# Optimization experiments

Measured on AMD Instinct MI355X. Metric: run time of the kernel, lower is better.

Reference implementation:

```python
import jax, jax.numpy as jnp
import numpy as np

EPS = 1e-6

def _log_g(x):
    # log of continuous g(x) = where(x>=0, x+0.5, sigmoid(x)) from minGRU paper
    return jnp.where(x >= 0, jnp.log(jax.nn.relu(x) + 0.5), -jax.nn.softplus(-x))

def setup_inputs() -> dict:
    key = jax.random.key(0)
    ks = jax.random.split(key, 4)
    B, S, D, E = 4, 2048, 1024, 8
    scale = D ** -0.5
    return {
        "inputs": jax.random.normal(ks[0], (B, S, D), dtype=jnp.float32),
        "norm_weight": jnp.ones((D,), jnp.float32),
        "router_w": jax.random.normal(ks[1], (E, D), jnp.float32) * scale,
        "router_b": jnp.zeros((E,), jnp.float32),
        "w_hg": jax.random.normal(ks[2], (E, 2 * D, D), jnp.float32) * scale,
        "w_out": jax.random.normal(ks[3], (E, D, D), jnp.float32) * scale,
    }

def reference(inputs, norm_weight, router_w, router_b, w_hg, w_out):
    D = inputs.shape[-1]
    # --- RMSNorm ---
    x = inputs * jax.lax.rsqrt(jnp.mean(inputs * inputs, axis=-1, keepdims=True) + EPS) * norm_weight
    # --- SMEAR: per-sample soft merge of expert weights via mean-pooled routing ---
    probs = jax.nn.softmax(jnp.mean(x, axis=1) @ router_w.T + router_b, axis=-1)  # [B,E]
    W_hg = jnp.einsum('be,ekd->bkd', probs, w_hg)    # [B,2D,D] merged to_hidden_and_gate
    W_out = jnp.einsum('be,eod->bod', probs, w_out)  # [B,D,D]  merged to_out
    # --- minGRU with merged weights (log-space parallel scan, no initial state) ---
    hg = jnp.einsum('bsd,bkd->bsk', x, W_hg)         # [B,S,2D]
    hidden, gate = hg[..., :D], hg[..., D:]
    log_coeffs = -jax.nn.softplus(gate)                      # log(1 - z_t)
    log_values = -jax.nn.softplus(-gate) + _log_g(hidden)    # log z_t + log g(h~_t)
    a_star = jnp.cumsum(log_coeffs, axis=1)
    log_h = a_star + jax.lax.cumlogsumexp(log_values - a_star, axis=1)
    h = jnp.exp(log_h)                               # [B,S,D] recurrent states
    new_state = h[:, -1:]                            # [B,1,D]
    out = jnp.einsum('bsk,bok->bso', h, W_out)       # proj_out
    aux_loss = jnp.zeros((), inputs.dtype)
    return (out + inputs, new_state, aux_loss)
```

## Files before the change

### kernel.cpp

```cpp
#include <hip/hip_runtime.h>
#include <hip/hip_bf16.h>
#include <hip/hip_fp16.h>

#define B_  4
#define S_  2048
#define D_  1024
#define E_  8
#define K2_ 2048

#define CHUNKS 64
#define CLEN   32

typedef __attribute__((ext_vector_type(8))) short short8;
typedef __attribute__((ext_vector_type(4))) float floatx4;

__device__ __forceinline__ void gld16(const void* g, const void* l) {
    __builtin_amdgcn_global_load_lds(
        (const __attribute__((address_space(1))) unsigned int*)g,
        (__attribute__((address_space(3))) unsigned int*)l, 16, 0, 0);
}

__device__ __forceinline__ unsigned short f2bf(float f) {
    unsigned int u = __float_as_uint(f);
    u += 0x7fffu + ((u >> 16) & 1u);
    return (unsigned short)(u >> 16);
}

__global__ void rmsnorm_k(const float* __restrict__ in, const float* __restrict__ nw,
                          __hip_bfloat16* __restrict__ x) {
    int b = blockIdx.y, s = blockIdx.x, t = threadIdx.x;
    const float4* row = (const float4*)(in + ((size_t)b * S_ + s) * D_);
    float4 v = row[t];
    float ss = v.x * v.x + v.y * v.y + v.z * v.z + v.w * v.w;
#pragma unroll
    for (int o = 32; o > 0; o >>= 1) ss += __shfl_down(ss, o, 64);
    __shared__ float ls[4];
    if ((t & 63) == 0) ls[t >> 6] = ss;
    __syncthreads();
    float tot = ls[0] + ls[1] + ls[2] + ls[3];
    float rs = rsqrtf(tot * (1.0f / (float)D_) + 1e-6f);
    float4 w = ((const float4*)nw)[t];
    ushort4 o;
    o.x = f2bf(v.x * rs * w.x); o.y = f2bf(v.y * rs * w.y);
    o.z = f2bf(v.z * rs * w.z); o.w = f2bf(v.w * rs * w.w);
    ((ushort4*)(x + ((size_t)b * S_ + s) * D_))[t] = o;
}

__global__ void xsum_k(const __hip_bfloat16* __restrict__ x, float* __restrict__ xs) {
    int d = blockIdx.x * 256 + threadIdx.x;
    int b = blockIdx.y;
    int s0 = blockIdx.z * 128;
    const __hip_bfloat16* p = x + ((size_t)b * S_ + s0) * D_ + d;
    float acc = 0.0f;
#pragma unroll 4
    for (int s = 0; s < 128; s++) { acc += __bfloat162float(*p); p += D_; }
    atomicAdd(&xs[b * D_ + d], acc);
}

__global__ void router_k(const float* __restrict__ xs, const float* __restrict__ rw,
                         const float* __restrict__ rb, float* __restrict__ probs,
                         float* __restrict__ aux) {
    int t = threadIdx.x;
    if (t == 255) *aux = 0.0f;
    int pair = t >> 3, sub = t & 7;
    int b = pair >> 3, e = pair & 7;
    float acc = 0.0f;
#pragma unroll 8
    for (int d = sub; d < D_; d += 8) acc += xs[b * D_ + d] * rw[e * D_ + d];
#pragma unroll
    for (int o = 4; o > 0; o >>= 1) acc += __shfl_down(acc, o, 8);
    __shared__ float lg[32];
    if (sub == 0) lg[pair] = acc * (1.0f / (float)S_) + rb[e];
    __syncthreads();
    if (t < 4) {
        float m = -1e30f;
        for (int e2 = 0; e2 < 8; e2++) m = fmaxf(m, lg[t * 8 + e2]);
        float ssum = 0.0f; float ex[8];
        for (int e2 = 0; e2 < 8; e2++) { ex[e2] = expf(lg[t * 8 + e2] - m); ssum += ex[e2]; }
        for (int e2 = 0; e2 < 8; e2++) probs[t * 8 + e2] = ex[e2] / ssum;
    }
}

__global__ void mix_k(const float* __restrict__ probs, const float* __restrict__ whg_e,
                      const float* __restrict__ wout_e, __hip_bfloat16* __restrict__ Whg,
                      __hip_bfloat16* __restrict__ Wout) {
    __shared__ float P[32];
    int t = threadIdx.x;
    if (t < 32) P[t] = probs[t];
    __syncthreads();
    size_t i4 = (size_t)blockIdx.x * 256 + t;
    const size_t T1q = (size_t)K2_ * D_ / 4;
    const size_t T2q = (size_t)D_ * D_ / 4;
    float4 a0 = {0,0,0,0}, a1 = {0,0,0,0}, a2 = {0,0,0,0}, a3 = {0,0,0,0};
    if (i4 < T1q) {
        const float4* src = (const float4*)whg_e;
#pragma unroll
        for (int e = 0; e < 8; e++) {
            float4 wv = src[(size_t)e * T1q + i4];
            float p0 = P[e], p1 = P[8 + e], p2 = P[16 + e], p3 = P[24 + e];
            a0.x += p0 * wv.x; a0.y += p0 * wv.y; a0.z += p0 * wv.z; a0.w += p0 * wv.w;
            a1.x += p1 * wv.x; a1.y += p1 * wv.y; a1.z += p1 * wv.z; a1.w += p1 * wv.w;
            a2.x += p2 * wv.x; a2.y += p2 * wv.y; a2.z += p2 * wv.z; a2.w += p2 * wv.w;
            a3.x += p3 * wv.x; a3.y += p3 * wv.y; a3.z += p3 * wv.z; a3.w += p3 * wv.w;
        }
        ushort4* dst = (ushort4*)Whg;
        ushort4 o;
        o.x = f2bf(a0.x); o.y = f2bf(a0.y); o.z = f2bf(a0.z); o.w = f2bf(a0.w);
        dst[0 * T1q + i4] = o;
        o.x = f2bf(a1.x); o.y = f2bf(a1.y); o.z = f2bf(a1.z); o.w = f2bf(a1.w);
        dst[1 * T1q + i4] = o;
        o.x = f2bf(a2.x); o.y = f2bf(a2.y); o.z = f2bf(a2.z); o.w = f2bf(a2.w);
        dst[2 * T1q + i4] = o;
        o.x = f2bf(a3.x); o.y = f2bf(a3.y); o.z = f2bf(a3.z); o.w = f2bf(a3.w);
        dst[3 * T1q + i4] = o;
    } else {
        size_t j4 = i4 - T1q;
        const float4* src = (const float4*)wout_e;
#pragma unroll
        for (int e = 0; e < 8; e++) {
            float4 wv = src[(size_t)e * T2q + j4];
            float p0 = P[e], p1 = P[8 + e], p2 = P[16 + e], p3 = P[24 + e];
            a0.x += p0 * wv.x; a0.y += p0 * wv.y; a0.z += p0 * wv.z; a0.w += p0 * wv.w;
            a1.x += p1 * wv.x; a1.y += p1 * wv.y; a1.z += p1 * wv.z; a1.w += p1 * wv.w;
            a2.x += p2 * wv.x; a2.y += p2 * wv.y; a2.z += p2 * wv.z; a2.w += p2 * wv.w;
            a3.x += p3 * wv.x; a3.y += p3 * wv.y; a3.z += p3 * wv.z; a3.w += p3 * wv.w;
        }
        ushort4* dst = (ushort4*)Wout;
        ushort4 o;
        o.x = f2bf(a0.x); o.y = f2bf(a0.y); o.z = f2bf(a0.z); o.w = f2bf(a0.w);
        dst[0 * T2q + j4] = o;
        o.x = f2bf(a1.x); o.y = f2bf(a1.y); o.z = f2bf(a1.z); o.w = f2bf(a1.w);
        dst[1 * T2q + j4] = o;
        o.x = f2bf(a2.x); o.y = f2bf(a2.y); o.z = f2bf(a2.z); o.w = f2bf(a2.w);
        dst[2 * T2q + j4] = o;
        o.x = f2bf(a3.x); o.y = f2bf(a3.y); o.z = f2bf(a3.z); o.w = f2bf(a3.w);
        dst[3 * T2q + j4] = o;
    }
}

__global__ __launch_bounds__(512, 2) void gemm_hg_cv(
    const __hip_bfloat16* __restrict__ A, const __hip_bfloat16* __restrict__ Bm,
    __half2* __restrict__ cv) {
    const int K = D_;
    int bz = blockIdx.z;
    A  += (size_t)bz * S_ * D_;
    Bm += (size_t)bz * K2_ * D_;
    __half2* CV = cv + (size_t)bz * S_ * D_;
    int id = blockIdx.x;
    int sw = (id & 7) * 8 + (id >> 3);
    int m0 = (sw >> 3) * 256, n0 = (sw & 7) * 128;
    __shared__ __hip_bfloat16 lA[2][2][256][32];
    __shared__ __hip_bfloat16 lBh[2][2][128][32];
    __shared__ __hip_bfloat16 lBg[2][2][128][32];
    int t = threadIdx.x;
    int w = t >> 6, lane = t & 63;
    int lm = lane & 15, quad = lane >> 4;
    int wr = w >> 1, wc = w & 1;
    floatx4 acch[4][4] = {};
    floatx4 accg[4][4] = {};
    int rloc = lane >> 2;
    int swz4 = ((lane & 3) ^ ((lane >> 3) & 3)) * 16;
    int pch  = (quad ^ ((lm >> 1) & 3)) * 16;

    const __hip_bfloat16* Bh = Bm;
    const __hip_bfloat16* Bg = Bm + (size_t)D_ * K;

    const char* pA0 = (const char*)(A  + (size_t)(m0 + (w * 2 + 0) * 16 + rloc) * K) + swz4;
    const char* pA1 = (const char*)(A  + (size_t)(m0 + (w * 2 + 1) * 16 + rloc) * K) + swz4;
    const char* pBhp = (const char*)(Bh + (size_t)(n0 + w * 16 + rloc) * K) + swz4;
    const char* pBgp = (const char*)(Bg + (size_t)(n0 + w * 16 + rloc) * K) + swz4;

    auto stage_kh0 = [&](int bb) {
        gld16(pA0, &lA[bb][0][(w * 2 + 0) * 16][0]);
        gld16(pA1, &lA[bb][0][(w * 2 + 1) * 16][0]);
        gld16(pBhp, &lBh[bb][0][w * 16][0]);
        gld16(pBgp, &lBg[bb][0][w * 16][0]);
    };
    auto stage_kh1 = [&](int bb) {
        gld16(pA0 + 64, &lA[bb][1][(w * 2 + 0) * 16][0]);
        gld16(pA1 + 64, &lA[bb][1][(w * 2 + 1) * 16][0]);
        gld16(pBhp + 64, &lBh[bb][1][w * 16][0]);
        gld16(pBgp + 64, &lBg[bb][1][w * 16][0]);
        pA0 += 128; pA1 += 128; pBhp += 128; pBgp += 128;
    };

    stage_kh0(0); stage_kh1(0);
    for (int kt = 0; kt < 16; kt++) {
        int cur = kt & 1, nxt = cur ^ 1;
        bool pre = (kt < 15);
        asm volatile("s_waitcnt vmcnt(4)" ::: "memory");
        __builtin_amdgcn_s_barrier();
        short8 af[4], bh0[2], bg0[2];
#pragma unroll
        for (int i = 0; i < 4; i++)
            af[i] = *(const short8*)((const char*)&lA[cur][0][wr * 64 + i * 16 + lm][0] + pch);
#pragma unroll
        for (int jj = 0; jj < 2; jj++) {
            bh0[jj] = *(const short8*)((const char*)&lBh[cur][0][wc * 64 + jj * 16 + lm][0] + pch);
            bg0[jj] = *(const short8*)((const char*)&lBg[cur][0][wc * 64 + jj * 16 + lm][0] + pch);
        }
        if (pre) stage_kh0(nxt);
        asm volatile("s_waitcnt lgkmcnt(0)" ::: "memory");
        __builtin_amdgcn_sched_barrier(0);
        __builtin_amdgcn_s_setprio(1);
#pragma unroll
        for (int i = 0; i < 4; i++)
#pragma unroll
            for (int jj = 0; jj < 2; jj++) {
                acch[i][jj] = __builtin_amdgcn_mfma_f32_16x16x32_bf16(af[i], bh0[jj], acch[i][jj], 0, 0, 0);
                accg[i][jj] = __builtin_amdgcn_mfma_f32_16x16x32_bf16(af[i], bg0[jj], accg[i][jj], 0, 0, 0);
            }
        __builtin_amdgcn_s_setprio(0);
        short8 bh1[2], bg1[2];
#pragma unroll
        for (int jj = 0; jj < 2; jj++) {
            bh1[jj] = *(const short8*)((const char*)&lBh[cur][0][wc * 64 + (jj + 2) * 16 + lm][0] + pch);
            bg1[jj] = *(const short8*)((const char*)&lBg[cur][0][wc * 64 + (jj + 2) * 16 + lm][0] + pch);
        }
        asm volatile("s_waitcnt lgkmcnt(0)" ::: "memory");
        __builtin_amdgcn_sched_barrier(0);
        __builtin_amdgcn_s_setprio(1);
#pragma unroll
        for (int i = 0; i < 4; i++)
#pragma unroll
            for (int jj = 0; jj < 2; jj++) {
                acch[i][jj + 2] = __builtin_amdgcn_mfma_f32_16x16x32_bf16(af[i], bh1[jj], acch[i][jj + 2], 0, 0, 0);
                accg[i][jj + 2] = __builtin_amdgcn_mfma_f32_16x16x32_bf16(af[i], bg1[jj], accg[i][jj + 2], 0, 0, 0);
            }
        __builtin_amdgcn_s_setprio(0);
        if (pre) asm volatile("s_waitcnt vmcnt(4)" ::: "memory");
        else     asm volatile("s_waitcnt vmcnt(0)" ::: "memory");
        __builtin_amdgcn_s_barrier();
        short8 a1f[4], bh2[2], bg2[2];
#pragma unroll
        for (int i = 0; i < 4; i++)
            a1f[i] = *(const short8*)((const char*)&lA[cur][1][wr * 64 + i * 16 + lm][0] + pch);
#pragma unroll
        for (int jj = 0; jj < 2; jj++) {
            bh2[jj] = *(const short8*)((const char*)&lBh[cur][1][wc * 64 + jj * 16 + lm][0] + pch);
            bg2[jj] = *(const short8*)((const char*)&lBg[cur][1][wc * 64 + jj * 16 + lm][0] + pch);
        }
        if (pre) stage_kh1(nxt);
        asm volatile("s_waitcnt lgkmcnt(0)" ::: "memory");
        __builtin_amdgcn_sched_barrier(0);
        __builtin_amdgcn_s_setprio(1);
#pragma unroll
        for (int i = 0; i < 4; i++)
#pragma unroll
            for (int jj = 0; jj < 2; jj++) {
                acch[i][jj] = __builtin_amdgcn_mfma_f32_16x16x32_bf16(a1f[i], bh2[jj], acch[i][jj], 0, 0, 0);
                accg[i][jj] = __builtin_amdgcn_mfma_f32_16x16x32_bf16(a1f[i], bg2[jj], accg[i][jj], 0, 0, 0);
            }
        __builtin_amdgcn_s_setprio(0);
        short8 bh3[2], bg3[2];
#pragma unroll
        for (int jj = 0; jj < 2; jj++) {
            bh3[jj] = *(const short8*)((const char*)&lBh[cur][1][wc * 64 + (jj + 2) * 16 + lm][0] + pch);
            bg3[jj] = *(const short8*)((const char*)&lBg[cur][1][wc * 64 + (jj + 2) * 16 + lm][0] + pch);
        }
        asm volatile("s_waitcnt lgkmcnt(0)" ::: "memory");
        __builtin_amdgcn_sched_barrier(0);
        __builtin_amdgcn_s_setprio(1);
#pragma unroll
        for (int i = 0; i < 4; i++)
#pragma unroll
            for (int jj = 0; jj < 2; jj++) {
                acch[i][jj + 2] = __builtin_amdgcn_mfma_f32_16x16x32_bf16(a1f[i], bh3[jj], acch[i][jj + 2], 0, 0, 0);
                accg[i][jj + 2] = __builtin_amdgcn_mfma_f32_16x16x32_bf16(a1f[i], bg3[jj], accg[i][jj + 2], 0, 0, 0);
            }
        __builtin_amdgcn_s_setprio(0);
    }
#pragma unroll
    for (int i = 0; i < 4; i++) {
#pragma unroll
        for (int j = 0; j < 4; j++) {
#pragma unroll
            for (int r = 0; r < 4; r++) {
                int m = m0 + wr * 64 + i * 16 + quad * 4 + r;
                int n = n0 + wc * 64 + j * 16 + lm;
                float hid = acch[i][j][r];
                float g   = accg[i][j][r];
                float eg  = expf(g);
                float c   = 1.0f / (1.0f + eg);
                float sg  = 1.0f - c;
                float gfn = (hid >= 0.0f) ? (hid + 0.5f)
                                          : (1.0f / (1.0f + expf(-hid)));
                CV[(size_t)m * D_ + n] = __floats2half2_rn(c, sg * gfn);
            }
        }
    }
}

__global__ __launch_bounds__(256) void gemm_bf16_bt(
    const __hip_bfloat16* __restrict__ A, const __hip_bfloat16* __restrict__ Bm,
    float* __restrict__ C, const float* __restrict__ R,
    int M, int N, int K, size_t sa, size_t sb, size_t sc, size_t sr) {
    int bz = blockIdx.z;
    A += (size_t)bz * sa; Bm += (size_t)bz * sb; C += (size_t)bz * sc;
    if (R) R += (size_t)bz * sr;
    int id = blockIdx.x;
    int sw = (id & 7) * 16 + (id >> 3);
    int m0 = (sw >> 3) * 128, n0 = (sw & 7) * 128;
    __shared__ __hip_bfloat16 lA[2][2][128][32];
    __shared__ __hip_bfloat16 lB[2][2][128][32];
    int t = threadIdx.x;
    int w = t >> 6, lane = t & 63;
    int lm = lane & 15, quad = lane >> 4;
    int wr = w >> 1, wc = w & 1;
    floatx4 acc[4][4] = {};
    int rloc = lane >> 2;
    int swz4 = ((lane & 3) ^ ((lane >> 3) & 3)) * 16;
    int pch  = (quad ^ ((lm >> 1) & 3)) * 16;

    const char* pA0 = (const char*)(A  + (size_t)(m0 + (w * 2 + 0) * 16 + rloc) * K) + swz4;
    const char* pA1 = (const char*)(A  + (size_t)(m0 + (w * 2 + 1) * 16 + rloc) * K) + swz4;
    const char* pB0 = (const char*)(Bm + (size_t)(n0 + (w * 2 + 0) * 16 + rloc) * K) + swz4;
    const char* pB1 = (const char*)(Bm + (size_t)(n0 + (w * 2 + 1) * 16 + rloc) * K) + swz4;

    auto stage_kh0 = [&](int bb) {
        gld16(pA0, &lA[bb][0][(w * 2 + 0) * 16][0]);
        gld16(pA1, &lA[bb][0][(w * 2 + 1) * 16][0]);
        gld16(pB0, &lB[bb][0][(w * 2 + 0) * 16][0]);
        gld16(pB1, &lB[bb][0][(w * 2 + 1) * 16][0]);
    };
    auto stage_kh1 = [&](int bb) {
        gld16(pA0 + 64, &lA[bb][1][(w * 2 + 0) * 16][0]);
        gld16(pA1 + 64, &lA[bb][1][(w * 2 + 1) * 16][0]);
        gld16(pB0 + 64, &lB[bb][1][(w * 2 + 0) * 16][0]);
        gld16(pB1 + 64, &lB[bb][1][(w * 2 + 1) * 16][0]);
        pA0 += 128; pA1 += 128; pB0 += 128; pB1 += 128;
    };

    stage_kh0(0); stage_kh1(0);
    int NT = K / 64;
    for (int kt = 0; kt < NT; kt++) {
        int cur = kt & 1, nxt = cur ^ 1;
        bool pre = (kt < NT - 1);
        asm volatile("s_waitcnt vmcnt(4)" ::: "memory");
        __builtin_amdgcn_s_barrier();
        short8 af[4], bf0[2];
#pragma unroll
        for (int i = 0; i < 4; i++)
            af[i] = *(const short8*)((const char*)&lA[cur][0][wr * 64 + i * 16 + lm][0] + pch);
#pragma unroll
        for (int jj = 0; jj < 2; jj++)
            bf0[jj] = *(const short8*)((const char*)&lB[cur][0][wc * 64 + jj * 16 + lm][0] + pch);
        if (pre) stage_kh0(nxt);
        asm volatile("s_waitcnt lgkmcnt(0)" ::: "memory");
        __builtin_amdgcn_sched_barrier(0);
        __builtin_amdgcn_s_setprio(1);
#pragma unroll
        for (int i = 0; i < 4; i++)
#pragma unroll
            for (int jj = 0; jj < 2; jj++)
                acc[i][jj] = __builtin_amdgcn_mfma_f32_16x16x32_bf16(af[i], bf0[jj], acc[i][jj], 0, 0, 0);
        __builtin_amdgcn_s_setprio(0);
        short8 bf1[2];
#pragma unroll
        for (int jj = 0; jj < 2; jj++)
            bf1[jj] = *(const short8*)((const char*)&lB[cur][0][wc * 64 + (jj + 2) * 16 + lm][0] + pch);
        asm volatile("s_waitcnt lgkmcnt(0)" ::: "memory");
        __builtin_amdgcn_sched_barrier(0);
        __builtin_amdgcn_s_setprio(1);
#pragma unroll
        for (int i = 0; i < 4; i++)
#pragma unroll
            for (int jj = 0; jj < 2; jj++)
                acc[i][jj + 2] = __builtin_amdgcn_mfma_f32_16x16x32_bf16(af[i], bf1[jj], acc[i][jj + 2], 0, 0, 0);
        __builtin_amdgcn_s_setprio(0);
        if (pre) asm volatile("s_waitcnt vmcnt(4)" ::: "memory");
        else     asm volatile("s_waitcnt vmcnt(0)" ::: "memory");
        __builtin_amdgcn_s_barrier();
        short8 a1f[4], bf2[2];
#pragma unroll
        for (int i = 0; i < 4; i++)
            a1f[i] = *(const short8*)((const char*)&lA[cur][1][wr * 64 + i * 16 + lm][0] + pch);
#pragma unroll
        for (int jj = 0; jj < 2; jj++)
            bf2[jj] = *(const short8*)((const char*)&lB[cur][1][wc * 64 + jj * 16 + lm][0] + pch);
        if (pre) stage_kh1(nxt);
        asm volatile("s_waitcnt lgkmcnt(0)" ::: "memory");
        __builtin_amdgcn_sched_barrier(0);
        __builtin_amdgcn_s_setprio(1);
#pragma unroll
        for (int i = 0; i < 4; i++)
#pragma unroll
            for (int jj = 0; jj < 2; jj++)
                acc[i][jj] = __builtin_amdgcn_mfma_f32_16x16x32_bf16(a1f[i], bf2[jj], acc[i][jj], 0, 0, 0);
        __builtin_amdgcn_s_setprio(0);
        short8 bf3[2];
#pragma unroll
        for (int jj = 0; jj < 2; jj++)
            bf3[jj] = *(const short8*)((const char*)&lB[cur][1][wc * 64 + (jj + 2) * 16 + lm][0] + pch);
        asm volatile("s_waitcnt lgkmcnt(0)" ::: "memory");
        __builtin_amdgcn_sched_barrier(0);
        __builtin_amdgcn_s_setprio(1);
#pragma unroll
        for (int i = 0; i < 4; i++)
#pragma unroll
            for (int jj = 0; jj < 2; jj++)
                acc[i][jj + 2] = __builtin_amdgcn_mfma_f32_16x16x32_bf16(a1f[i], bf3[jj], acc[i][jj + 2], 0, 0, 0);
        __builtin_amdgcn_s_setprio(0);
    }
#pragma unroll
    for (int i = 0; i < 4; i++) {
#pragma unroll
        for (int j = 0; j < 4; j++) {
#pragma unroll
            for (int r = 0; r < 4; r++) {
                int m = m0 + wr * 64 + i * 16 + quad * 4 + r;
                int n = n0 + wc * 64 + j * 16 + lm;
                float v = acc[i][j][r];
                if (R) v += R[(size_t)m * N + n];
                __builtin_nontemporal_store(v, &C[(size_t)m * N + n]);
            }
        }
    }
}

__global__ void scanA_k(const __half2* __restrict__ cv, float* __restrict__ Cc,
                        float* __restrict__ Vc) {
    int c = blockIdx.x, b = blockIdx.y, t = threadIdx.x;
    const float4* p = (const float4*)(cv + (size_t)(b * S_ + c * CLEN) * D_) + t;
    float P0 = 1, P1 = 1, P2 = 1, P3 = 1;
    float V0 = 0, V1 = 0, V2 = 0, V3 = 0;
#pragma unroll 4
    for (int s = 0; s < CLEN; s++) {
        float4 raw = p[(size_t)s * (D_ / 4)];
        const __half2* e = (const __half2*)&raw;
        float c0 = __low2float(e[0]), v0 = __high2float(e[0]);
        float c1 = __low2float(e[1]), v1 = __high2float(e[1]);
        float c2 = __low2float(e[2]), v2 = __high2float(e[2]);
        float c3 = __low2float(e[3]), v3 = __high2float(e[3]);
        P0 *= c0; V0 = fmaf(c0, V0, v0);
        P1 *= c1; V1 = fmaf(c1, V1, v1);
        P2 *= c2; V2 = fmaf(c2, V2, v2);
        P3 *= c3; V3 = fmaf(c3, V3, v3);
    }
    size_t q = ((size_t)(b * CHUNKS + c)) * (D_ / 4) + t;
    ((float4*)Cc)[q] = make_float4(P0, P1, P2, P3);
    ((float4*)Vc)[q] = make_float4(V0, V1, V2, V3);
}

__global__ void scanC_k(const __half2* __restrict__ cv, const float* __restrict__ Cc,
                        const float* __restrict__ Vc,
                        __hip_bfloat16* __restrict__ hout, float* __restrict__ ns) {
    int c = blockIdx.x, b = blockIdx.y, t = threadIdx.x;
    float h0 = 0, h1 = 0, h2 = 0, h3 = 0;
#pragma unroll 4
    for (int cc = 0; cc < c; cc++) {
        size_t q = ((size_t)(b * CHUNKS + cc)) * (D_ / 4) + t;
        float4 C4 = ((const float4*)Cc)[q];
        float4 V4 = ((const float4*)Vc)[q];
        h0 = fmaf(C4.x, h0, V4.x); h1 = fmaf(C4.y, h1, V4.y);
        h2 = fmaf(C4.z, h2, V4.z); h3 = fmaf(C4.w, h3, V4.w);
    }
    const float4* p = (const float4*)(cv + (size_t)(b * S_ + c * CLEN) * D_) + t;
    ushort4* hq = (ushort4*)(hout + (size_t)(b * S_ + c * CLEN) * D_) + t;
#pragma unroll 4
    for (int s = 0; s < CLEN; s++) {
        float4 raw = p[(size_t)s * (D_ / 4)];
        const __half2* e = (const __half2*)&raw;
        h0 = fmaf(__low2float(e[0]), h0, __high2float(e[0]));
        h1 = fmaf(__low2float(e[1]), h1, __high2float(e[1]));
        h2 = fmaf(__low2float(e[2]), h2, __high2float(e[2]));
        h3 = fmaf(__low2float(e[3]), h3, __high2float(e[3]));
        ushort4 o;
        o.x = f2bf(h0); o.y = f2bf(h1); o.z = f2bf(h2); o.w = f2bf(h3);
        hq[(size_t)s * (D_ / 4)] = o;
    }
    if (c == CHUNKS - 1)
        ((float4*)(ns + (size_t)b * D_))[t] = make_float4(h0, h1, h2, h3);
}

extern "C" void kernel_launch(void* const* d_in, const int* in_sizes, int n_in,
                              void* d_out_v, int out_size, void* d_ws, size_t ws_size,
                              hipStream_t stream) {
    const float* inputs = (const float*)d_in[0];
    const float* nw     = (const float*)d_in[1];
    const float* rw     = (const float*)d_in[2];
    const float* rb     = (const float*)d_in[3];
    const float* whg_e  = (const float*)d_in[4];
    const float* wout_e = (const float*)d_in[5];
    float* out = (float*)d_out_v;

    float* ws = (float*)d_ws;
    __half2*        cv      = (__half2*)ws;
    __hip_bfloat16* x_bf    = (__hip_bfloat16*)(ws + 8388608);
    __hip_bfloat16* h_bf    = (__hip_bfloat16*)(ws + 12582912);
    __hip_bfloat16* Whg_bf  = (__hip_bfloat16*)(ws + 16777216);
    __hip_bfloat16* Wout_bf = (__hip_bfloat16*)(ws + 20971520);
    float* xsum  = ws + 23068672;
    float* probs = ws + 23072768;
    float* Cc    = ws + 23072800;
    float* Vc    = ws + 23334944;

    hipMemsetAsync(xsum, 0, (size_t)B_ * D_ * sizeof(float), stream);

    rmsnorm_k<<<dim3(S_, B_), 256, 0, stream>>>(inputs, nw, x_bf);
    xsum_k<<<dim3(D_ / 256, B_, 16), 256, 0, stream>>>(x_bf, xsum);
    router_k<<<1, 256, 0, stream>>>(xsum, rw, rb, probs,
                                    out + (size_t)B_ * S_ * D_ + (size_t)B_ * D_);
    mix_k<<<3072, 256, 0, stream>>>(probs, whg_e, wout_e, Whg_bf, Wout_bf);

    gemm_hg_cv<<<dim3(64, 1, B_), 512, 0, stream>>>(x_bf, Whg_bf, cv);

    scanA_k<<<dim3(CHUNKS, B_), 256, 0, stream>>>(cv, Cc, Vc);
    scanC_k<<<dim3(CHUNKS, B_), 256, 0, stream>>>(
        cv, Cc, Vc, h_bf, out + (size_t)B_ * S_ * D_);

    gemm_bf16_bt<<<dim3(128, 1, B_), 256, 0, stream>>>(
        h_bf, Wout_bf, out, inputs, S_, D_, D_,
        (size_t)S_ * D_, (size_t)D_ * D_, (size_t)S_ * D_, (size_t)S_ * D_);
}
```

Baseline: 304.4 us.

## Enlarge out-projection GEMM tile to 256x128 with 512 threads, simplify LDS-read scheduling

The output GEMM moves from 128x128 tiles with 256 threads to 256x128 tiles with 512 threads. Each workgroup stages one B row-slice per wave and two A slices, so B reuse goes up and the grid halves. In both GEMMs, the split LDS-fragment loads with explicit lgkmcnt waits and sched_barriers are replaced by one load of all fragments per K half, followed by a single 32-MFMA (or 16-MFMA) burst. This leaves instruction interleaving to the compiler, at the cost of higher register pressure and fewer workgroups (256) than CUs times occupancy might ideally want.

```diff
diff --git a/kernel.cpp b/kernel.cpp
--- a/kernel.cpp
+++ b/kernel.cpp
@@ -190,85 +190,53 @@
         bool pre = (kt < 15);
         asm volatile("s_waitcnt vmcnt(4)" ::: "memory");
         __builtin_amdgcn_s_barrier();
-        short8 af[4], bh0[2], bg0[2];
-#pragma unroll
-        for (int i = 0; i < 4; i++)
-            af[i] = *(const short8*)((const char*)&lA[cur][0][wr * 64 + i * 16 + lm][0] + pch);
-#pragma unroll
-        for (int jj = 0; jj < 2; jj++) {
-            bh0[jj] = *(const short8*)((const char*)&lBh[cur][0][wc * 64 + jj * 16 + lm][0] + pch);
-            bg0[jj] = *(const short8*)((const char*)&lBg[cur][0][wc * 64 + jj * 16 + lm][0] + pch);
-        }
-        if (pre) stage_kh0(nxt);
-        asm volatile("s_waitcnt lgkmcnt(0)" ::: "memory");
-        __builtin_amdgcn_sched_barrier(0);
-        __builtin_amdgcn_s_setprio(1);
-#pragma unroll
-        for (int i = 0; i < 4; i++)
-#pragma unroll
-            for (int jj = 0; jj < 2; jj++) {
-                acch[i][jj] = __builtin_amdgcn_mfma_f32_16x16x32_bf16(af[i], bh0[jj], acch[i][jj], 0, 0, 0);
-                accg[i][jj] = __builtin_amdgcn_mfma_f32_16x16x32_bf16(af[i], bg0[jj], accg[i][jj], 0, 0, 0);
+        asm volatile("" ::: "memory");
+        {
+            short8 af[4], bh[4], bg[4];
+#pragma unroll
+            for (int i = 0; i < 4; i++)
+                af[i] = *(const short8*)((const char*)&lA[cur][0][wr * 64 + i * 16 + lm][0] + pch);
+#pragma unroll
+            for (int j = 0; j < 4; j++) {
+                bh[j] = *(const short8*)((const char*)&lBh[cur][0][wc * 64 + j * 16 + lm][0] + pch);
+                bg[j] = *(const short8*)((const char*)&lBg[cur][0][wc * 64 + j * 16 + lm][0] + pch);
             }
-        __builtin_amdgcn_s_setprio(0);
-        short8 bh1[2], bg1[2];
-#pragma unroll
-        for (int jj = 0; jj < 2; jj++) {
-            bh1[jj] = *(const short8*)((const char*)&lBh[cur][0][wc * 64 + (jj + 2) * 16 + lm][0] + pch);
-            bg1[jj] = *(const short8*)((const char*)&lBg[cur][0][wc * 64 + (jj + 2) * 16 + lm][0] + pch);
-        }
-        asm volatile("s_waitcnt lgkmcnt(0)" ::: "memory");
-        __builtin_amdgcn_sched_barrier(0);
-        __builtin_amdgcn_s_setprio(1);
-#pragma unroll
-        for (int i = 0; i < 4; i++)
-#pragma unroll
-            for (int jj = 0; jj < 2; jj++) {
-                acch[i][jj + 2] = __builtin_amdgcn_mfma_f32_16x16x32_bf16(af[i], bh1[jj], acch[i][jj + 2], 0, 0, 0);
-                accg[i][jj + 2] = __builtin_amdgcn_mfma_f32_16x16x32_bf16(af[i], bg1[jj], accg[i][jj + 2], 0, 0, 0);
-            }
-        __builtin_amdgcn_s_setprio(0);
+            if (pre) stage_kh0(nxt);
+            __builtin_amdgcn_s_setprio(1);
+#pragma unroll
+            for (int i = 0; i < 4; i++)
+#pragma unroll
+                for (int j = 0; j < 4; j++) {
+                    acch[i][j] = __builtin_amdgcn_mfma_f32_16x16x32_bf16(af[i], bh[j], acch[i][j], 0, 0, 0);
+                    accg[i][j] = __builtin_amdgcn_mfma_f32_16x16x32_bf16(af[i], bg[j], accg[i][j], 0, 0, 0);
+                }
+            __builtin_amdgcn_s_setprio(0);
+        }
         if (pre) asm volatile("s_waitcnt vmcnt(4)" ::: "memory");
         else     asm volatile("s_waitcnt vmcnt(0)" ::: "memory");
         __builtin_amdgcn_s_barrier();
-        short8 a1f[4], bh2[2], bg2[2];
-#pragma unroll
-        for (int i = 0; i < 4; i++)
-            a1f[i] = *(const short8*)((const char*)&lA[cur][1][wr * 64 + i * 16 + lm][0] + pch);
-#pragma unroll
-        for (int jj = 0; jj < 2; jj++) {
-            bh2[jj] = *(const short8*)((const char*)&lBh[cur][1][wc * 64 + jj * 16 + lm][0] + pch);
-            bg2[jj] = *(const short8*)((const char*)&lBg[cur][1][wc * 64 + jj * 16 + lm][0] + pch);
-        }
-        if (pre) stage_kh1(nxt);
-        asm volatile("s_waitcnt lgkmcnt(0)" ::: "memory");
-        __builtin_amdgcn_sched_barrier(0);
-        __builtin_amdgcn_s_setprio(1);
-#pragma unroll
-        for (int i = 0; i < 4; i++)
-#pragma unroll
-            for (int jj = 0; jj < 2; jj++) {
-                acch[i][jj] = __builtin_amdgcn_mfma_f32_16x16x32_bf16(a1f[i], bh2[jj], acch[i][jj], 0, 0, 0);
-                accg[i][jj] = __builtin_amdgcn_mfma_f32_16x16x32_bf16(a1f[i], bg2[jj], accg[i][jj], 0, 0, 0);
+        asm volatile("" ::: "memory");
+        {
+            short8 af[4], bh[4], bg[4];
+#pragma unroll
+            for (int i = 0; i < 4; i++)
+                af[i] = *(const short8*)((const char*)&lA[cur][1][wr * 64 + i * 16 + lm][0] + pch);
+#pragma unroll
+            for (int j = 0; j < 4; j++) {
+                bh[j] = *(const short8*)((const char*)&lBh[cur][1][wc * 64 + j * 16 + lm][0] + pch);
+                bg[j] = *(const short8*)((const char*)&lBg[cur][1][wc * 64 + j * 16 + lm][0] + pch);
             }
-        __builtin_amdgcn_s_setprio(0);
-        short8 bh3[2], bg3[2];
-#pragma unroll
-        for (int jj = 0; jj < 2; jj++) {
-            bh3[jj] = *(const short8*)((const char*)&lBh[cur][1][wc * 64 + (jj + 2) * 16 + lm][0] + pch);
-            bg3[jj] = *(const short8*)((const char*)&lBg[cur][1][wc * 64 + (jj + 2) * 16 + lm][0] + pch);
-        }
-        asm volatile("s_waitcnt lgkmcnt(0)" ::: "memory");
-        __builtin_amdgcn_sched_barrier(0);
-        __builtin_amdgcn_s_setprio(1);
-#pragma unroll
-        for (int i = 0; i < 4; i++)
-#pragma unroll
-            for (int jj = 0; jj < 2; jj++) {
-                acch[i][jj + 2] = __builtin_amdgcn_mfma_f32_16x16x32_bf16(a1f[i], bh3[jj], acch[i][jj + 2], 0, 0, 0);
-                accg[i][jj + 2] = __builtin_amdgcn_mfma_f32_16x16x32_bf16(a1f[i], bg3[jj], accg[i][jj + 2], 0, 0, 0);
-            }
-        __builtin_amdgcn_s_setprio(0);
+            if (pre) stage_kh1(nxt);
+            __builtin_amdgcn_s_setprio(1);
+#pragma unroll
+            for (int i = 0; i < 4; i++)
+#pragma unroll
+                for (int j = 0; j < 4; j++) {
+                    acch[i][j] = __builtin_amdgcn_mfma_f32_16x16x32_bf16(af[i], bh[j], acch[i][j], 0, 0, 0);
+                    accg[i][j] = __builtin_amdgcn_mfma_f32_16x16x32_bf16(af[i], bg[j], accg[i][j], 0, 0, 0);
+                }
+            __builtin_amdgcn_s_setprio(0);
+        }
     }
 #pragma unroll
     for (int i = 0; i < 4; i++) {
@@ -291,7 +259,7 @@
     }
 }
 
-__global__ __launch_bounds__(256) void gemm_bf16_bt(
+__global__ __launch_bounds__(512, 2) void gemm_bf16_bt(
     const __hip_bfloat16* __restrict__ A, const __hip_bfloat16* __restrict__ Bm,
     float* __restrict__ C, const float* __restrict__ R,
     int M, int N, int K, size_t sa, size_t sb, size_t sc, size_t sr) {
@@ -299,9 +267,9 @@
     A += (size_t)bz * sa; Bm += (size_t)bz * sb; C += (size_t)bz * sc;
     if (R) R += (size_t)bz * sr;
     int id = blockIdx.x;
-    int sw = (id & 7) * 16 + (id >> 3);
-    int m0 = (sw >> 3) * 128, n0 = (sw & 7) * 128;
-    __shared__ __hip_bfloat16 lA[2][2][128][32];
+    int sw = (id & 7) * 8 + (id >> 3);
+    int m0 = (sw >> 3) * 256, n0 = (sw & 7) * 128;
+    __shared__ __hip_bfloat16 lA[2][2][256][32];
     __shared__ __hip_bfloat16 lB[2][2][128][32];
     int t = threadIdx.x;
     int w = t >> 6, lane = t & 63;
@@ -314,21 +282,18 @@
 
     const char* pA0 = (const char*)(A  + (size_t)(m0 + (w * 2 + 0) * 16 + rloc) * K) + swz4;
     const char* pA1 = (const char*)(A  + (size_t)(m0 + (w * 2 + 1) * 16 + rloc) * K) + swz4;
-    const char* pB0 = (const char*)(Bm + (size_t)(n0 + (w * 2 + 0) * 16 + rloc) * K) + swz4;
-    const char* pB1 = (const char*)(Bm + (size_t)(n0 + (w * 2 + 1) * 16 + rloc) * K) + swz4;
+    const char* pB0 = (const char*)(Bm + (size_t)(n0 + w * 16 + rloc) * K) + swz4;
 
     auto stage_kh0 = [&](int bb) {
         gld16(pA0, &lA[bb][0][(w * 2 + 0) * 16][0]);
         gld16(pA1, &lA[bb][0][(w * 2 + 1) * 16][0]);
-        gld16(pB0, &lB[bb][0][(w * 2 + 0) * 16][0]);
-        gld16(pB1, &lB[bb][0][(w * 2 + 1) * 16][0]);
+        gld16(pB0, &lB[bb][0][w * 16][0]);
     };
     auto stage_kh1 = [&](int bb) {
         gld16(pA0 + 64, &lA[bb][1][(w * 2 + 0) * 16][0]);
         gld16(pA1 + 64, &lA[bb][1][(w * 2 + 1) * 16][0]);
-        gld16(pB0 + 64, &lB[bb][1][(w * 2 + 0) * 16][0]);
-        gld16(pB1 + 64, &lB[bb][1][(w * 2 + 1) * 16][0]);
-        pA0 += 128; pA1 += 128; pB0 += 128; pB1 += 128;
+        gld16(pB0 + 64, &lB[bb][1][w * 16][0]);
+        pA0 += 128; pA1 += 128; pB0 += 128;
     };
 
     stage_kh0(0); stage_kh1(0);
@@ -336,71 +301,47 @@
     for (int kt = 0; kt < NT; kt++) {
         int cur = kt & 1, nxt = cur ^ 1;
         bool pre = (kt < NT - 1);
-        asm volatile("s_waitcnt vmcnt(4)" ::: "memory");
+        asm volatile("s_waitcnt vmcnt(3)" ::: "memory");
         __builtin_amdgcn_s_barrier();
-        short8 af[4], bf0[2];
-#pragma unroll
-        for (int i = 0; i < 4; i++)
-            af[i] = *(const short8*)((const char*)&lA[cur][0][wr * 64 + i * 16 + lm][0] + pch);
-#pragma unroll
-        for (int jj = 0; jj < 2; jj++)
-            bf0[jj] = *(const short8*)((const char*)&lB[cur][0][wc * 64 + jj * 16 + lm][0] + pch);
-        if (pre) stage_kh0(nxt);
-        asm volatile("s_waitcnt lgkmcnt(0)" ::: "memory");
-        __builtin_amdgcn_sched_barrier(0);
-        __builtin_amdgcn_s_setprio(1);
-#pragma unroll
-        for (int i = 0; i < 4; i++)
-#pragma unroll
-            for (int jj = 0; jj < 2; jj++)
-                acc[i][jj] = __builtin_amdgcn_mfma_f32_16x16x32_bf16(af[i], bf0[jj], acc[i][jj], 0, 0, 0);
-        __builtin_amdgcn_s_setprio(0);
-        short8 bf1[2];
-#pragma unroll
-        for (int jj = 0; jj < 2; jj++)
-            bf1[jj] = *(const short8*)((const char*)&lB[cur][0][wc * 64 + (jj + 2) * 16 + lm][0] + pch);
-        asm volatile("s_waitcnt lgkmcnt(0)" ::: "memory");
-        __builtin_amdgcn_sched_barrier(0);
-        __builtin_amdgcn_s_setprio(1);
-#pragma unroll
-        for (int i = 0; i < 4; i++)
-#pragma unroll
-            for (int jj = 0; jj < 2; jj++)
-                acc[i][jj + 2] = __builtin_amdgcn_mfma_f32_16x16x32_bf16(af[i], bf1[jj], acc[i][jj + 2], 0, 0, 0);
-        __builtin_amdgcn_s_setprio(0);
-        if (pre) asm volatile("s_waitcnt vmcnt(4)" ::: "memory");
+        asm volatile("" ::: "memory");
+        {
+            short8 af[4], bf[4];
+#pragma unroll
+            for (int i = 0; i < 4; i++)
+                af[i] = *(const short8*)((const char*)&lA[cur][0][wr * 64 + i * 16 + lm][0] + pch);
+#pragma unroll
+            for (int j = 0; j < 4; j++)
+                bf[j] = *(const short8*)((const char*)&lB[cur][0][wc * 64 + j * 16 + lm][0] + pch);
+            if (pre) stage_kh0(nxt);
+            __builtin_amdgcn_s_setprio(1);
+#pragma unroll
+            for (int i = 0; i < 4; i++)
+#pragma unroll
+                for (int j = 0; j < 4; j++)
+                    acc[i][j] = __builtin_amdgcn_mfma_f32_16x16x32_bf16(af[i], bf[j], acc[i][j], 0, 0, 0);
+            __builtin_amdgcn_s_setprio(0);
+        }
+        if (pre) asm volatile("s_waitcnt vmcnt(3)" ::: "memory");
         else     asm volatile("s_waitcnt vmcnt(0)" ::: "memory");
         __builtin_amdgcn_s_barrier();
-        short8 a1f[4], bf2[2];
-#pragma unroll
-        for (int i = 0; i < 4; i++)
-            a1f[i] = *(const short8*)((const char*)&lA[cur][1][wr * 64 + i * 16 + lm][0] + pch);
-#pragma unroll
-        for (int jj = 0; jj < 2; jj++)
-            bf2[jj] = *(const short8*)((const char*)&lB[cur][1][wc * 64 + jj * 16 + lm][0] + pch);
-        if (pre) stage_kh1(nxt);
-        asm volatile("s_waitcnt lgkmcnt(0)" ::: "memory");
-        __builtin_amdgcn_sched_barrier(0);
-        __builtin_amdgcn_s_setprio(1);
-#pragma unroll
-        for (int i = 0; i < 4; i++)
-#pragma unroll
-            for (int jj = 0; jj < 2; jj++)
-                acc[i][jj] = __builtin_amdgcn_mfma_f32_16x16x32_bf16(a1f[i], bf2[jj], acc[i][jj], 0, 0, 0);
-        __builtin_amdgcn_s_setprio(0);
-        short8 bf3[2];
-#pragma unroll
-        for (int jj = 0; jj < 2; jj++)
-            bf3[jj] = *(const short8*)((const char*)&lB[cur][1][wc * 64 + (jj + 2) * 16 + lm][0] + pch);
-        asm volatile("s_waitcnt lgkmcnt(0)" ::: "memory");
-        __builtin_amdgcn_sched_barrier(0);
-        __builtin_amdgcn_s_setprio(1);
-#pragma unroll
-        for (int i = 0; i < 4; i++)
-#pragma unroll
-            for (int jj = 0; jj < 2; jj++)
-                acc[i][jj + 2] = __builtin_amdgcn_mfma_f32_16x16x32_bf16(a1f[i], bf3[jj], acc[i][jj + 2], 0, 0, 0);
-        __builtin_amdgcn_s_setprio(0);
+        asm volatile("" ::: "memory");
+        {
+            short8 af[4], bf[4];
+#pragma unroll
+            for (int i = 0; i < 4; i++)
+                af[i] = *(const short8*)((const char*)&lA[cur][1][wr * 64 + i * 16 + lm][0] + pch);
+#pragma unroll
+            for (int j = 0; j < 4; j++)
+                bf[j] = *(const short8*)((const char*)&lB[cur][1][wc * 64 + j * 16 + lm][0] + pch);
+            if (pre) stage_kh1(nxt);
+            __builtin_amdgcn_s_setprio(1);
+#pragma unroll
+            for (int i = 0; i < 4; i++)
+#pragma unroll
+                for (int j = 0; j < 4; j++)
+                    acc[i][j] = __builtin_amdgcn_mfma_f32_16x16x32_bf16(af[i], bf[j], acc[i][j], 0, 0, 0);
+            __builtin_amdgcn_s_setprio(0);
+        }
     }
 #pragma unroll
     for (int i = 0; i < 4; i++) {
@@ -509,7 +450,7 @@
     scanC_k<<<dim3(CHUNKS, B_), 256, 0, stream>>>(
         cv, Cc, Vc, h_bf, out + (size_t)B_ * S_ * D_);
 
-    gemm_bf16_bt<<<dim3(128, 1, B_), 256, 0, stream>>>(
+    gemm_bf16_bt<<<dim3(64, 1, B_), 512, 0, stream>>>(
         h_bf, Wout_bf, out, inputs, S_, D_, D_,
         (size_t)S_ * D_, (size_t)D_ * D_, (size_t)S_ * D_, (size_t)S_ * D_);
 }
```

New measurement: 295.3 us. -3.0%, faster.
